# Kernel tuning notes

Measured on AMD Instinct MI355X. Metric: run time of the kernel, lower is better.

Reference implementation:

```python
import jax, jax.numpy as jnp
import numpy as np

BATCH, IN_DIM, HID, OUT_DIM, Z = 8192, 2048, 4096, 2048, 4
CONN_P = 0.5  # Bernoulli keep-probability y


def random_activation(h, ids):
    # ids: [dim] int32 in [0,5); per-channel nonlinearity applied over batch.
    ids = ids[None, :]
    return jnp.select(
        [ids == 0, ids == 1, ids == 2, ids == 3],
        [jax.nn.relu(h), jax.nn.sigmoid(h), jnp.tanh(h), jnp.where(h >= 0, h, 0.1 * h)],
        jax.nn.selu(h),
    )


def _make_linear(key, fan_in, fan_out):
    kw, kb, km = jax.random.split(key, 3)
    w = jax.random.normal(kw, (fan_out, fan_in), dtype=jnp.float32)
    mask = jax.random.bernoulli(km, CONN_P, (fan_out, fan_in)).astype(jnp.float32)
    b = jax.random.normal(kb, (fan_out,), dtype=jnp.float32)
    return w * mask, b


def setup_inputs() -> dict:
    key = jax.random.key(0)
    ks = jax.random.split(key, 16)
    inp = {"input_pattern": jax.random.normal(ks[0], (BATCH, IN_DIM), dtype=jnp.float32)}
    dims = [(IN_DIM, HID)] + [(HID, HID)] * Z + [(HID, OUT_DIM)]  # z+2 Linear layers
    for i, (fi, fo) in enumerate(dims):
        w, b = _make_linear(ks[1 + i], fi, fo)
        inp[f"w{i}"] = w
        inp[f"b{i}"] = b
        inp[f"ids{i}"] = jax.random.randint(ks[8 + i], (fo,), 0, 5, dtype=jnp.int32)
    return inp


def reference(input_pattern, w0, b0, ids0, w1, b1, ids1, w2, b2, ids2,
              w3, b3, ids3, w4, b4, ids4, w5, b5, ids5):
    ws = (w0, w1, w2, w3, w4, w5)
    bs = (b0, b1, b2, b3, b4, b5)
    ids = (ids0, ids1, ids2, ids3, ids4, ids5)
    h = input_pattern
    for w, b, i in zip(ws, bs, ids):
        h = random_activation(h @ w.T + b, i)
    return h
```

## Files before the change

### kernel.cpp

```cpp
#include <hip/hip_runtime.h>

typedef _Float16 f16;
typedef _Float16 f16x8 __attribute__((ext_vector_type(8)));
typedef float f32x4 __attribute__((ext_vector_type(4)));

__device__ __forceinline__ void gload_lds16(const void* g, void* l) {
  __builtin_amdgcn_global_load_lds(
      (const __attribute__((address_space(1))) void*)g,
      (__attribute__((address_space(3))) void*)l, 16, 0, 0);
}

__device__ __forceinline__ float act_apply(float x, int id) {
  switch (id) {
    case 0: return fmaxf(x, 0.0f);
    case 1: return 1.0f / (1.0f + __expf(-x));
    case 2: return tanhf(x);
    case 3: return x >= 0.0f ? x : 0.1f * x;
    default: return 1.0507009873554805f *
                    (x > 0.0f ? x : 1.6732632423543772f * expm1f(x));
  }
}

template <bool FINAL>
__global__ __launch_bounds__(512, 2)
void gemm256(const f16* __restrict__ A, const f16* __restrict__ W,
             const float* __restrict__ bias, const int* __restrict__ ids,
             float Sa, float invSn, void* __restrict__ outv,
             int M, int N, int K) {
  __shared__ f16 lA[4][256 * 32];
  __shared__ f16 lB[4][256 * 32];

  const int tid  = (int)threadIdx.x;
  const int lane = tid & 63;
  const int wid  = tid >> 6;
  const int wm   = wid >> 2;
  const int wn   = wid & 3;

  const int nbx = N >> 8;
  const int nwg = (M >> 8) * nbx;
  const int b   = (int)blockIdx.x;
  const int swz = (b & 7) * (nwg >> 3) + (b >> 3);
  const int brow = (swz / nbx) << 8;
  const int bcol = (swz % nbx) << 8;

  const int d0 = tid << 4;
  const int d1 = d0 + 8192;
  const int s0 = d0 ^ (((d0 >> 7) & 7) << 4);
  const int s1 = d1 ^ (((d1 >> 7) & 7) << 4);
  const int r0 = s0 >> 6, c0 = (s0 >> 4) & 3;
  const int r1 = s1 >> 6, c1 = (s1 >> 4) & 3;

  const f16* pA0 = A + (long)(brow + r0) * K + c0 * 8;
  const f16* pA1 = A + (long)(brow + r1) * K + c1 * 8;
  const f16* pB0 = W + (long)(bcol + r0) * K + c0 * 8;
  const f16* pB1 = W + (long)(bcol + r1) * K + c1 * 8;
  const int e0 = tid << 3;
  const int e1 = e0 + 4096;

  const int fr = lane & 15;
  const int kb = lane >> 4;
  const int xorv = ((fr >> 1) & 7) << 4;
  const char* baA = (const char*)&lA[0][0];
  const char* baB = (const char*)&lB[0][0];

  int offA[8], offB[4];
#pragma unroll
  for (int m = 0; m < 8; ++m)
    offA[m] = (((wm * 128 + m * 16 + fr) << 6) + (kb << 4)) ^ xorv;
#pragma unroll
  for (int n = 0; n < 4; ++n)
    offB[n] = (((wn * 64 + n * 16 + fr) << 6) + (kb << 4)) ^ xorv;

  f32x4 acc[8][4];
#pragma unroll
  for (int m = 0; m < 8; ++m)
#pragma unroll
    for (int n = 0; n < 4; ++n) acc[m][n] = (f32x4){0.f, 0.f, 0.f, 0.f};

  const int nt = K >> 5;

#pragma unroll
  for (int t = 0; t < 3; ++t) {
    const long kk = (long)t << 5;
    gload_lds16(pA0 + kk, &lA[t][e0]);
    gload_lds16(pA1 + kk, &lA[t][e1]);
    gload_lds16(pB0 + kk, &lB[t][e0]);
    gload_lds16(pB1 + kk, &lB[t][e1]);
  }
  asm volatile("s_waitcnt vmcnt(4)" ::: "memory");
  __builtin_amdgcn_s_barrier();
  asm volatile("" ::: "memory");

  f16x8 aC[4], bC[4], aN[4], bN[4], aL[4];
#pragma unroll
  for (int m = 0; m < 4; ++m) aC[m] = *(const f16x8*)(baA + offA[m]);
#pragma unroll
  for (int n = 0; n < 4; ++n) bC[n] = *(const f16x8*)(baB + offB[n]);

#define BODY(U, AC, BC, AN, BN)                                            \
  do {                                                                     \
    const int so  = ((U) & 3) << 14;                                       \
    const int son = (((U) + 1) & 3) << 14;                                 \
    _Pragma("unroll")                                                      \
    for (int m = 0; m < 4; ++m)                                            \
      aL[m] = *(const f16x8*)(baA + so + offA[m + 4]);                     \
    if ((U) + 1 < nt) {                                                    \
      _Pragma("unroll")                                                    \
      for (int m = 0; m < 4; ++m)                                          \
        AN[m] = *(const f16x8*)(baA + son + offA[m]);                      \
      _Pragma("unroll")                                                    \
      for (int n = 0; n < 4; ++n)                                          \
        BN[n] = *(const f16x8*)(baB + son + offB[n]);                      \
    }                                                                      \
    {                                                                      \
      const int ps  = ((U) + 3 < nt) ? (U) + 3 : nt - 1;                   \
      const int pso = ps & 3;                                              \
      const long kk = (long)ps << 5;                                       \
      gload_lds16(pA0 + kk, &lA[pso][e0]);                                 \
      gload_lds16(pA1 + kk, &lA[pso][e1]);                                 \
      gload_lds16(pB0 + kk, &lB[pso][e0]);                                 \
      gload_lds16(pB1 + kk, &lB[pso][e1]);                                 \
    }                                                                      \
    __builtin_amdgcn_s_setprio(1);                                         \
    _Pragma("unroll")                                                      \
    for (int m = 0; m < 4; ++m)                                            \
      _Pragma("unroll")                                                    \
      for (int n = 0; n < 4; ++n)                                          \
        acc[m][n] = __builtin_amdgcn_mfma_f32_16x16x32_f16(                \
            AC[m], BC[n], acc[m][n], 0, 0, 0);                             \
    _Pragma("unroll")                                                      \
    for (int m = 0; m < 4; ++m)                                            \
      _Pragma("unroll")                                                    \
      for (int n = 0; n < 4; ++n)                                          \
        acc[4 + m][n] = __builtin_amdgcn_mfma_f32_16x16x32_f16(            \
            aL[m], BC[n], acc[4 + m][n], 0, 0, 0);                         \
    __builtin_amdgcn_s_setprio(0);                                         \
    if ((U) < nt - 1) {                                                    \
      asm volatile("s_waitcnt vmcnt(4)" ::: "memory");                     \
      __builtin_amdgcn_s_barrier();                                        \
      asm volatile("" ::: "memory");                                       \
    }                                                                      \
  } while (0)

  for (int s = 0; s < nt; s += 2) {
    BODY(s, aC, bC, aN, bN);
    BODY(s + 1, aN, bN, aC, bC);
  }
#undef BODY
  asm volatile("s_waitcnt vmcnt(0)" ::: "memory");

  const int r4 = (lane >> 4) << 2;
#pragma unroll
  for (int n = 0; n < 4; ++n) {
    const int gcol = bcol + wn * 64 + n * 16 + fr;
    const float bv = bias[gcol];
    const int id   = ids[gcol];
#pragma unroll
    for (int m = 0; m < 8; ++m) {
      const int grow = brow + wm * 128 + m * 16 + r4;
#pragma unroll
      for (int i = 0; i < 4; ++i) {
        const float y = act_apply(acc[m][n][i] * Sa + bv, id);
        if (FINAL) {
          ((float*)outv)[(long)(grow + i) * N + gcol] = y;
        } else {
          ((f16*)outv)[(long)(grow + i) * N + gcol] = (f16)(y * invSn);
        }
      }
    }
  }
}

template <bool FINAL>
__global__ __launch_bounds__(256, 4)
void gemm128(const f16* __restrict__ A, const f16* __restrict__ W,
             const float* __restrict__ bias, const int* __restrict__ ids,
             float Sa, float invSn, void* __restrict__ outv,
             int M, int N, int K) {
  __shared__ f16 lA[2][128 * 32];
  __shared__ f16 lB[2][128 * 32];

  const int tid  = (int)threadIdx.x;
  const int lane = tid & 63;
  const int wid  = tid >> 6;
  const int wr   = (wid >> 1) * 64;
  const int wc   = (wid & 1) * 64;

  const int nbx = N >> 7;
  const int nwg = (M >> 7) * nbx;
  const int b   = (int)blockIdx.x;
  const int swz = (b & 7) * (nwg >> 3) + (b >> 3);
  const int brow = (swz / nbx) << 7;
  const int bcol = (swz % nbx) << 7;

  const int d0 = tid << 4;
  const int d1 = d0 + 4096;
  const int s0 = d0 ^ (((d0 >> 7) & 7) << 4);
  const int s1 = d1 ^ (((d1 >> 7) & 7) << 4);
  const int r0 = s0 >> 6, c0 = (s0 >> 4) & 3;
  const int r1 = s1 >> 6, c1 = (s1 >> 4) & 3;

  const f16* pA0 = A + (long)(brow + r0) * K + c0 * 8;
  const f16* pA1 = A + (long)(brow + r1) * K + c1 * 8;
  const f16* pB0 = W + (long)(bcol + r0) * K + c0 * 8;
  const f16* pB1 = W + (long)(bcol + r1) * K + c1 * 8;
  const int e0 = tid << 3;
  const int e1 = e0 + 2048;

  const int fr = lane & 15;
  const int kb = lane >> 4;
  const int xorv = ((fr >> 1) & 7) << 4;

  int offA[4], offB[4];
#pragma unroll
  for (int m = 0; m < 4; ++m)
    offA[m] = (((wr + m * 16 + fr) << 6) + (kb << 4)) ^ xorv;
#pragma unroll
  for (int n = 0; n < 4; ++n)
    offB[n] = (((wc + n * 16 + fr) << 6) + (kb << 4)) ^ xorv;

  f32x4 acc[4][4];
#pragma unroll
  for (int m = 0; m < 4; ++m)
#pragma unroll
    for (int n = 0; n < 4; ++n) acc[m][n] = (f32x4){0.f, 0.f, 0.f, 0.f};

  const int nt = K >> 5;
  int buf = 0;

  gload_lds16(pA0, &lA[0][e0]);
  gload_lds16(pA1, &lA[0][e1]);
  gload_lds16(pB0, &lB[0][e0]);
  gload_lds16(pB1, &lB[0][e1]);
  __syncthreads();

  for (int t = 0; t < nt; ++t) {
    if (t + 1 < nt) {
      const long kk = (long)(t + 1) << 5;
      gload_lds16(pA0 + kk, &lA[buf ^ 1][e0]);
      gload_lds16(pA1 + kk, &lA[buf ^ 1][e1]);
      gload_lds16(pB0 + kk, &lB[buf ^ 1][e0]);
      gload_lds16(pB1 + kk, &lB[buf ^ 1][e1]);
    }
    const char* bA = (const char*)&lA[buf][0];
    const char* bB = (const char*)&lB[buf][0];
    f16x8 af[4], bf[4];
#pragma unroll
    for (int m = 0; m < 4; ++m) af[m] = *(const f16x8*)(bA + offA[m]);
#pragma unroll
    for (int n = 0; n < 4; ++n) bf[n] = *(const f16x8*)(bB + offB[n]);
#pragma unroll
    for (int m = 0; m < 4; ++m)
#pragma unroll
      for (int n = 0; n < 4; ++n)
        acc[m][n] = __builtin_amdgcn_mfma_f32_16x16x32_f16(af[m], bf[n],
                                                           acc[m][n], 0, 0, 0);
    if (t + 1 < nt) {
      __syncthreads();
      buf ^= 1;
    }
  }

  const int r4 = (lane >> 4) << 2;
#pragma unroll
  for (int n = 0; n < 4; ++n) {
    const int gcol = bcol + wc + n * 16 + fr;
    const float bv = bias[gcol];
    const int id   = ids[gcol];
#pragma unroll
    for (int m = 0; m < 4; ++m) {
      const int grow = brow + wr + m * 16 + r4;
#pragma unroll
      for (int i = 0; i < 4; ++i) {
        const float y = act_apply(acc[m][n][i] * Sa + bv, id);
        if (FINAL) {
          ((float*)outv)[(long)(grow + i) * N + gcol] = y;
        } else {
          ((f16*)outv)[(long)(grow + i) * N + gcol] = (f16)(y * invSn);
        }
      }
    }
  }
}

__global__ void cvt_f32_to_f16(const float* __restrict__ in, f16* __restrict__ out,
                               float scale, int n) {
  int i = ((int)blockIdx.x * 256 + (int)threadIdx.x) * 8;
  const int stride = (int)gridDim.x * 256 * 8;
  for (; i < n; i += stride) {
    const float4 v0 = *(const float4*)(in + i);
    const float4 v1 = *(const float4*)(in + i + 4);
    f16x8 h;
    h[0] = (f16)(v0.x * scale); h[1] = (f16)(v0.y * scale);
    h[2] = (f16)(v0.z * scale); h[3] = (f16)(v0.w * scale);
    h[4] = (f16)(v1.x * scale); h[5] = (f16)(v1.y * scale);
    h[6] = (f16)(v1.z * scale); h[7] = (f16)(v1.w * scale);
    *(f16x8*)(out + i) = h;
  }
}

extern "C" void kernel_launch(void* const* d_in, const int* in_sizes, int n_in,
                              void* d_out, int out_size, void* d_ws, size_t ws_size,
                              hipStream_t stream) {
  (void)in_sizes; (void)n_in; (void)out_size; (void)ws_size;
  const int M = 8192, IND = 2048, HID = 4096, OUTD = 2048;
  const float* x = (const float*)d_in[0];

  f16* actA = (f16*)d_ws;
  f16* actB = actA + (size_t)M * HID;
  f16* wbuf = actB + (size_t)M * HID;

  const float S[6] = {1.f, 16.f, 512.f, 16384.f, 262144.f, 8388608.f};
  const int Ks[6] = {IND, HID, HID, HID, HID, HID};
  const int Ns[6] = {HID, HID, HID, HID, HID, OUTD};

  cvt_f32_to_f16<<<2048, 256, 0, stream>>>(x, actA, 1.0f, M * IND);

  f16* cur = actA;
  f16* nxt = actB;
  for (int i = 0; i < 6; ++i) {
    const int K = Ks[i], N = Ns[i];
    const float* w  = (const float*)d_in[1 + 3 * i];
    const float* bs = (const float*)d_in[2 + 3 * i];
    const int* id   = (const int*)d_in[3 + 3 * i];

    cvt_f32_to_f16<<<2048, 256, 0, stream>>>(w, wbuf, 1.0f, N * K);

    if (i < 3) {
      const int nblk = (M >> 8) * (N >> 8);
      gemm256<false><<<nblk, 512, 0, stream>>>(
          cur, wbuf, bs, id, S[i], 1.0f / S[i + 1], nxt, M, N, K);
      f16* t = cur; cur = nxt; nxt = t;
    } else if (i < 5) {
      const int nblk = (M >> 7) * (N >> 7);
      gemm128<false><<<nblk, 256, 0, stream>>>(
          cur, wbuf, bs, id, S[i], 1.0f / S[i + 1], nxt, M, N, K);
      f16* t = cur; cur = nxt; nxt = t;
    } else {
      const int nblk = (M >> 7) * (N >> 7);
      gemm128<true><<<nblk, 256, 0, stream>>>(
          cur, wbuf, bs, id, S[i], 1.0f, d_out, M, N, K);
    }
  }
}
```

Baseline: 1.943 ms.

## Replace 8-wave 256x256 GEMM with 4-wave kernel using 128x128 warp tiles

The 256x256 block GEMM used for the first three layers now runs with 4 waves (256 threads), each computing a 128x128 sub-tile (8x8 MFMA fragments) instead of 8 waves at 128x64. Each thread issues twice as many global-to-LDS loads per stage. The explicit register double-buffering of LDS fragments and the setprio hints are dropped in favour of a simple per-iteration load-then-MFMA loop. The goal is more MFMA work per LDS read, but the larger accumulator set raises register pressure to one block per CU and gives less latency hiding.

```diff
diff --git a/kernel.cpp b/kernel.cpp
--- a/kernel.cpp
+++ b/kernel.cpp
@@ -22,19 +22,19 @@
 }
 
 template <bool FINAL>
-__global__ __launch_bounds__(512, 2)
-void gemm256(const f16* __restrict__ A, const f16* __restrict__ W,
-             const float* __restrict__ bias, const int* __restrict__ ids,
-             float Sa, float invSn, void* __restrict__ outv,
-             int M, int N, int K) {
+__global__ __launch_bounds__(256, 1)
+void gemm_fat(const f16* __restrict__ A, const f16* __restrict__ W,
+              const float* __restrict__ bias, const int* __restrict__ ids,
+              float Sa, float invSn, void* __restrict__ outv,
+              int M, int N, int K) {
   __shared__ f16 lA[4][256 * 32];
   __shared__ f16 lB[4][256 * 32];
 
   const int tid  = (int)threadIdx.x;
   const int lane = tid & 63;
   const int wid  = tid >> 6;
-  const int wm   = wid >> 2;
-  const int wn   = wid & 3;
+  const int wr   = (wid >> 1) << 7;
+  const int wc   = (wid & 1) << 7;
 
   const int nbx = N >> 8;
   const int nwg = (M >> 8) * nbx;
@@ -43,19 +43,30 @@
   const int brow = (swz / nbx) << 8;
   const int bcol = (swz % nbx) << 8;
 
-  const int d0 = tid << 4;
-  const int d1 = d0 + 8192;
-  const int s0 = d0 ^ (((d0 >> 7) & 7) << 4);
-  const int s1 = d1 ^ (((d1 >> 7) & 7) << 4);
-  const int r0 = s0 >> 6, c0 = (s0 >> 4) & 3;
-  const int r1 = s1 >> 6, c1 = (s1 >> 4) & 3;
-
-  const f16* pA0 = A + (long)(brow + r0) * K + c0 * 8;
-  const f16* pA1 = A + (long)(brow + r1) * K + c1 * 8;
-  const f16* pB0 = W + (long)(bcol + r0) * K + c0 * 8;
-  const f16* pB1 = W + (long)(bcol + r1) * K + c1 * 8;
-  const int e0 = tid << 3;
-  const int e1 = e0 + 4096;
+  const f16* pA[4];
+  const f16* pB[4];
+  int edst[4];
+#pragma unroll
+  for (int c = 0; c < 4; ++c) {
+    const int d = (tid << 4) + c * 4096;
+    const int s = d ^ (((d >> 7) & 7) << 4);
+    const int row = s >> 6, colb = (s >> 4) & 3;
+    pA[c] = A + (long)(brow + row) * K + colb * 8;
+    pB[c] = W + (long)(bcol + row) * K + colb * 8;
+    edst[c] = (tid << 3) + c * 2048;
+  }
+
+#define STAGE(T)                                     \
+  do {                                               \
+    const int _sl = (T) & 3;                         \
+    const long _k = (long)(T) << 5;                  \
+    _Pragma("unroll")                                \
+    for (int c = 0; c < 4; ++c)                      \
+      gload_lds16(pA[c] + _k, &lA[_sl][edst[c]]);    \
+    _Pragma("unroll")                                \
+    for (int c = 0; c < 4; ++c)                      \
+      gload_lds16(pB[c] + _k, &lB[_sl][edst[c]]);    \
+  } while (0)
 
   const int fr = lane & 15;
   const int kb = lane >> 4;
@@ -63,101 +74,65 @@
   const char* baA = (const char*)&lA[0][0];
   const char* baB = (const char*)&lB[0][0];
 
-  int offA[8], offB[4];
+  int offA[8], offB[8];
 #pragma unroll
   for (int m = 0; m < 8; ++m)
-    offA[m] = (((wm * 128 + m * 16 + fr) << 6) + (kb << 4)) ^ xorv;
-#pragma unroll
-  for (int n = 0; n < 4; ++n)
-    offB[n] = (((wn * 64 + n * 16 + fr) << 6) + (kb << 4)) ^ xorv;
-
-  f32x4 acc[8][4];
+    offA[m] = (((wr + m * 16 + fr) << 6) + (kb << 4)) ^ xorv;
+#pragma unroll
+  for (int n = 0; n < 8; ++n)
+    offB[n] = (((wc + n * 16 + fr) << 6) + (kb << 4)) ^ xorv;
+
+  f32x4 acc[8][8];
 #pragma unroll
   for (int m = 0; m < 8; ++m)
 #pragma unroll
-    for (int n = 0; n < 4; ++n) acc[m][n] = (f32x4){0.f, 0.f, 0.f, 0.f};
+    for (int n = 0; n < 8; ++n) acc[m][n] = (f32x4){0.f, 0.f, 0.f, 0.f};
 
   const int nt = K >> 5;
 
-#pragma unroll
-  for (int t = 0; t < 3; ++t) {
-    const long kk = (long)t << 5;
-    gload_lds16(pA0 + kk, &lA[t][e0]);
-    gload_lds16(pA1 + kk, &lA[t][e1]);
-    gload_lds16(pB0 + kk, &lB[t][e0]);
-    gload_lds16(pB1 + kk, &lB[t][e1]);
-  }
-  asm volatile("s_waitcnt vmcnt(4)" ::: "memory");
+  STAGE(0);
+  STAGE(1);
+  STAGE(2);
+  asm volatile("s_waitcnt vmcnt(16)" ::: "memory");
   __builtin_amdgcn_s_barrier();
   asm volatile("" ::: "memory");
 
-  f16x8 aC[4], bC[4], aN[4], bN[4], aL[4];
-#pragma unroll
-  for (int m = 0; m < 4; ++m) aC[m] = *(const f16x8*)(baA + offA[m]);
-#pragma unroll
-  for (int n = 0; n < 4; ++n) bC[n] = *(const f16x8*)(baB + offB[n]);
-
-#define BODY(U, AC, BC, AN, BN)                                            \
-  do {                                                                     \
-    const int so  = ((U) & 3) << 14;                                       \
-    const int son = (((U) + 1) & 3) << 14;                                 \
-    _Pragma("unroll")                                                      \
-    for (int m = 0; m < 4; ++m)                                            \
-      aL[m] = *(const f16x8*)(baA + so + offA[m + 4]);                     \
-    if ((U) + 1 < nt) {                                                    \
-      _Pragma("unroll")                                                    \
-      for (int m = 0; m < 4; ++m)                                          \
-        AN[m] = *(const f16x8*)(baA + son + offA[m]);                      \
-      _Pragma("unroll")                                                    \
-      for (int n = 0; n < 4; ++n)                                          \
-        BN[n] = *(const f16x8*)(baB + son + offB[n]);                      \
-    }                                                                      \
-    {                                                                      \
-      const int ps  = ((U) + 3 < nt) ? (U) + 3 : nt - 1;                   \
-      const int pso = ps & 3;                                              \
-      const long kk = (long)ps << 5;                                       \
-      gload_lds16(pA0 + kk, &lA[pso][e0]);                                 \
-      gload_lds16(pA1 + kk, &lA[pso][e1]);                                 \
-      gload_lds16(pB0 + kk, &lB[pso][e0]);                                 \
-      gload_lds16(pB1 + kk, &lB[pso][e1]);                                 \
-    }                                                                      \
-    __builtin_amdgcn_s_setprio(1);                                         \
-    _Pragma("unroll")                                                      \
-    for (int m = 0; m < 4; ++m)                                            \
-      _Pragma("unroll")                                                    \
-      for (int n = 0; n < 4; ++n)                                          \
-        acc[m][n] = __builtin_amdgcn_mfma_f32_16x16x32_f16(                \
-            AC[m], BC[n], acc[m][n], 0, 0, 0);                             \
-    _Pragma("unroll")                                                      \
-    for (int m = 0; m < 4; ++m)                                            \
-      _Pragma("unroll")                                                    \
-      for (int n = 0; n < 4; ++n)                                          \
-        acc[4 + m][n] = __builtin_amdgcn_mfma_f32_16x16x32_f16(            \
-            aL[m], BC[n], acc[4 + m][n], 0, 0, 0);                         \
-    __builtin_amdgcn_s_setprio(0);                                         \
-    if ((U) < nt - 1) {                                                    \
-      asm volatile("s_waitcnt vmcnt(4)" ::: "memory");                     \
-      __builtin_amdgcn_s_barrier();                                        \
-      asm volatile("" ::: "memory");                                       \
-    }                                                                      \
-  } while (0)
-
-  for (int s = 0; s < nt; s += 2) {
-    BODY(s, aC, bC, aN, bN);
-    BODY(s + 1, aN, bN, aC, bC);
-  }
-#undef BODY
+  for (int u = 0; u < nt; ++u) {
+    const int so = (u & 3) << 14;
+    const int ps = (u + 3 < nt) ? (u + 3) : (nt - 1);
+    STAGE(ps);
+
+    f16x8 af[8], bf[8];
+#pragma unroll
+    for (int m = 0; m < 8; ++m) af[m] = *(const f16x8*)(baA + so + offA[m]);
+#pragma unroll
+    for (int n = 0; n < 8; ++n) bf[n] = *(const f16x8*)(baB + so + offB[n]);
+
+#pragma unroll
+    for (int m = 0; m < 8; ++m)
+#pragma unroll
+      for (int n = 0; n < 8; ++n)
+        acc[m][n] = __builtin_amdgcn_mfma_f32_16x16x32_f16(af[m], bf[n],
+                                                           acc[m][n], 0, 0, 0);
+
+    if (u < nt - 1) {
+      asm volatile("s_waitcnt vmcnt(16)" ::: "memory");
+      __builtin_amdgcn_s_barrier();
+      asm volatile("" ::: "memory");
+    }
+  }
+#undef STAGE
   asm volatile("s_waitcnt vmcnt(0)" ::: "memory");
 
   const int r4 = (lane >> 4) << 2;
 #pragma unroll
-  for (int n = 0; n < 4; ++n) {
-    const int gcol = bcol + wn * 64 + n * 16 + fr;
+  for (int n = 0; n < 8; ++n) {
+    const int gcol = bcol + wc + n * 16 + fr;
     const float bv = bias[gcol];
     const int id   = ids[gcol];
 #pragma unroll
     for (int m = 0; m < 8; ++m) {
-      const int grow = brow + wm * 128 + m * 16 + r4;
+      const int grow = brow + wr + m * 16 + r4;
 #pragma unroll
       for (int i = 0; i < 4; ++i) {
         const float y = act_apply(acc[m][n][i] * Sa + bv, id);
@@ -328,7 +303,7 @@
 
     if (i < 3) {
       const int nblk = (M >> 8) * (N >> 8);
-      gemm256<false><<<nblk, 512, 0, stream>>>(
+      gemm_fat<false><<<nblk, 256, 0, stream>>>(
           cur, wbuf, bs, id, S[i], 1.0f / S[i + 1], nxt, M, N, K);
       f16* t = cur; cur = nxt; nxt = t;
     } else if (i < 5) {
```

Result: slower. 2.832 ms (+45.8%).
